# Kernel tuning notes

Hardware: AMD Instinct MI355X
Metric: run time of the kernel (lower is better)

## Reference

```python
import jax, jax.numpy as jnp
import numpy as np

DIM = 1024
HEADS = 16
HD = DIM // HEADS            # 64
MLP = 4 * DIM                # 4096
IN_OUT = MLP + 3 * DIM       # 7168, in_proj out dim
OUT_IN = MLP + DIM           # 5120, out_proj in dim
OUT_OUT = 2 * DIM            # 2048, out_proj out dim
R = 2                        # residual PQ levels
K = 64                       # codebook size
NCB = HEADS                  # num_codebooks = num_heads * codebooks_ratio
IN_CLUSTERS = HEADS * (IN_OUT // DIM)                 # 112
OUT_CLUSTERS = HEADS * max(1, OUT_OUT // OUT_IN)      # 16
SUB_IN = DIM // NCB          # 64
SUB_OUT = OUT_IN // NCB      # 320
EPS = 1e-5


def setup_inputs() -> dict:
    key = jax.random.key(0)
    k1, k2, k3, k4, k5 = jax.random.split(key, 5)
    B, N = 4, 1024
    x = jax.random.normal(k1, (B, N, DIM), jnp.float32)
    in_codebooks = jax.random.normal(k2, (R, IN_CLUSTERS, NCB, K, SUB_IN), jnp.float32) * 0.02
    in_indices = jax.random.randint(k3, (R, IN_OUT, NCB), 0, K, jnp.int32)
    out_codebooks = jax.random.normal(k4, (R, OUT_CLUSTERS, NCB, K, SUB_OUT), jnp.float32) * 0.02
    out_indices = jax.random.randint(k5, (R, OUT_OUT, NCB), 0, K, jnp.int32)
    return {"x": x, "in_codebooks": in_codebooks, "in_indices": in_indices,
            "out_codebooks": out_codebooks, "out_indices": out_indices}


def _decode_weight(cb, idx):
    """Decode RPQ weight. cb: (R, n_clusters, n_codebooks, K, sub), idx: (R, O, n_codebooks).
    Returns dense weight (O, n_codebooks*sub)."""
    Rr, nclust, C, _, sub = cb.shape
    O = idx.shape[1]
    cluster = jnp.arange(O) // (O // nclust)                       # per-row cluster id
    w = cb[jnp.arange(Rr)[:, None, None],
           cluster[None, :, None],
           jnp.arange(C)[None, None, :],
           idx]                                                    # (R, O, C, sub)
    return w.sum(0).reshape(O, C * sub)


def reference(x, in_codebooks, in_indices, out_codebooks, out_indices):
    B, N, C = x.shape
    res = x
    # LayerNorm without affine
    mu = x.mean(-1, keepdims=True)
    var = x.var(-1, keepdims=True)
    xn = (x - mu) * jax.lax.rsqrt(var + EPS)
    # in_proj: dequant + GEMM
    Win = _decode_weight(in_codebooks, in_indices)                 # (IN_OUT, DIM)
    h = jnp.einsum('bnc,oc->bno', xn, Win)                         # (B, N, IN_OUT)
    xm, q, k, v = jnp.split(h, [MLP, MLP + DIM, MLP + 2 * DIM], axis=-1)
    q = q.reshape(B, N, HEADS, HD).transpose(0, 2, 1, 3)
    k = k.reshape(B, N, HEADS, HD).transpose(0, 2, 1, 3)
    v = v.reshape(B, N, HEADS, HD).transpose(0, 2, 1, 3)
    scale = HD ** -0.5
    attn = jax.nn.softmax(jnp.einsum('bhqd,bhkd->bhqk', q, k) * scale, axis=-1)
    xa = jnp.einsum('bhqk,bhkd->bhqd', attn, v).transpose(0, 2, 1, 3).reshape(B, N, C)
    # out_proj: dequant + GEMM on concatenated [mlp, attn]
    Wout = _decode_weight(out_codebooks, out_indices)              # (OUT_OUT, OUT_IN)
    o = jnp.einsum('bnc,oc->bno', jnp.concatenate([xm, xa], axis=-1), Wout)
    x_mlp, x_attn = o[..., :DIM], o[..., DIM:]
    return x_mlp + x_attn + res
```

## Files before the change

### kernel.cpp

```cpp
#include <hip/hip_runtime.h>
#include <hip/hip_bf16.h>

typedef float f32x4 __attribute__((ext_vector_type(4)));
typedef short short8 __attribute__((ext_vector_type(8)));

#define LDH 7168
#define MFMA16(d, x, y) d = __builtin_amdgcn_mfma_f32_16x16x32_bf16(x, y, d, 0, 0, 0)

__device__ __forceinline__ void async_ld16(const void* g, void* l) {
  __builtin_amdgcn_global_load_lds(
      (const __attribute__((address_space(1))) unsigned int*)g,
      (__attribute__((address_space(3))) unsigned int*)l, 16, 0, 0);
}

__device__ __forceinline__ float bf2f(unsigned short u) {
  union { unsigned int i; float f; } c; c.i = ((unsigned int)u) << 16; return c.f;
}

__device__ __forceinline__ ushort4 pack_bf16x4(float4 v) {
  ushort4 u;
  __hip_bfloat16 b;
  b = __float2bfloat16(v.x); u.x = *(unsigned short*)&b;
  b = __float2bfloat16(v.y); u.y = *(unsigned short*)&b;
  b = __float2bfloat16(v.z); u.z = *(unsigned short*)&b;
  b = __float2bfloat16(v.w); u.w = *(unsigned short*)&b;
  return u;
}

__global__ __launch_bounds__(256) void decode_win_k(const float* __restrict__ cb,
                                                    const int* __restrict__ idx,
                                                    __hip_bfloat16* __restrict__ Win) {
  const int o = blockIdx.x;
  const int cluster = o >> 6;
  const int c = threadIdx.x >> 4;
  const int s4 = (threadIdx.x & 15) * 4;
  const int k0 = idx[o * 16 + c];
  const int k1 = idx[(7168 + o) * 16 + c];
  const float4 v0 = *(const float4*)&cb[((((size_t)cluster) * 16 + c) * 64 + k0) * 64 + s4];
  const float4 v1 = *(const float4*)&cb[((((size_t)(112 + cluster)) * 16 + c) * 64 + k1) * 64 + s4];
  float4 v; v.x = v0.x + v1.x; v.y = v0.y + v1.y; v.z = v0.z + v1.z; v.w = v0.w + v1.w;
  *(ushort4*)&Win[(size_t)o * 1024 + c * 64 + s4] = pack_bf16x4(v);
}

__global__ __launch_bounds__(256) void decode_weff_k(const float* __restrict__ cb,
                                                     const int* __restrict__ idx,
                                                     __hip_bfloat16* __restrict__ W) {
  const int o = blockIdx.x;
  const int cl1 = o >> 7, cl2 = cl1 + 8;
  for (int e4 = threadIdx.x * 4; e4 < 5120; e4 += 1024) {
    const int c = e4 / 320, s = e4 - c * 320;
    float4 acc = {0.f, 0.f, 0.f, 0.f};
    #pragma unroll
    for (int r = 0; r < 2; ++r) {
      const int ka = idx[((size_t)r * 2048 + o) * 16 + c];
      const int kb = idx[((size_t)r * 2048 + o + 1024) * 16 + c];
      const float4 va = *(const float4*)&cb[((((size_t)r * 16 + cl1) * 16 + c) * 64 + ka) * 320 + s];
      const float4 vb = *(const float4*)&cb[((((size_t)r * 16 + cl2) * 16 + c) * 64 + kb) * 320 + s];
      acc.x += va.x + vb.x; acc.y += va.y + vb.y; acc.z += va.z + vb.z; acc.w += va.w + vb.w;
    }
    *(ushort4*)&W[(size_t)o * 5120 + e4] = pack_bf16x4(acc);
  }
}

__global__ __launch_bounds__(256) void ln_k(const float* __restrict__ x,
                                            __hip_bfloat16* __restrict__ xn) {
  const int row = blockIdx.x;
  const float4 v = ((const float4*)(x + (size_t)row * 1024))[threadIdx.x];
  float s = v.x + v.y + v.z + v.w;
  float s2 = v.x * v.x + v.y * v.y + v.z * v.z + v.w * v.w;
  #pragma unroll
  for (int off = 32; off > 0; off >>= 1) {
    s += __shfl_down(s, off, 64);
    s2 += __shfl_down(s2, off, 64);
  }
  __shared__ float red[8];
  if ((threadIdx.x & 63) == 0) { red[threadIdx.x >> 6] = s; red[4 + (threadIdx.x >> 6)] = s2; }
  __syncthreads();
  s = red[0] + red[1] + red[2] + red[3];
  s2 = red[4] + red[5] + red[6] + red[7];
  const float mu = s * (1.f / 1024.f);
  const float rstd = rsqrtf(s2 * (1.f / 1024.f) - mu * mu + 1e-5f);
  float4 nv;
  nv.x = (v.x - mu) * rstd; nv.y = (v.y - mu) * rstd;
  nv.z = (v.z - mu) * rstd; nv.w = (v.w - mu) * rstd;
  *(ushort4*)(xn + (size_t)row * 1024 + threadIdx.x * 4) = pack_bf16x4(nv);
}

__global__ __launch_bounds__(512, 2) void gemm1_k(const __hip_bfloat16* __restrict__ A,
                                                  const __hip_bfloat16* __restrict__ B,
                                                  __hip_bfloat16* __restrict__ C,
                                                  __hip_bfloat16* __restrict__ vT) {
  __shared__ ushort sm[65536];
  const int tid = threadIdx.x;
  const int lane = tid & 63, wid = tid >> 6;
  const int g = lane >> 4, r16 = lane & 15;
  const int wr = wid >> 2, wc = wid & 3;

  const int x = blockIdx.x & 7, local = blockIdx.x >> 3;
  const int mb = (x >> 1) * 4 + local / 14;
  const int nb = (x & 1) * 14 + local % 14;
  const int m0 = mb * 256, n0 = nb * 256;

  auto stageA = [&](int kt, int base) {
    #pragma unroll
    for (int i = 0; i < 4; ++i) {
      const int c = i * 512 + tid;
      const int lc = c ^ (((c >> 5) & 1) << 1);
      const int row = lc >> 3, col = (lc & 7) * 8;
      async_ld16(&A[(size_t)(m0 + row) * 1024 + kt * 64 + col], &sm[base + c * 8]);
    }
  };
  auto stageB = [&](int kt, int base) {
    #pragma unroll
    for (int i = 0; i < 4; ++i) {
      const int c = i * 512 + tid;
      const int lc = c ^ (((c >> 5) & 1) << 1);
      const int row = lc >> 3, col = (lc & 7) * 8;
      async_ld16(&B[(size_t)(n0 + row) * 1024 + kt * 64 + col], &sm[base + 16384 + c * 8]);
    }
  };
  auto rdA = [&](int base, int mm, int kk) -> short8 {
    const int row = wr * 128 + mm * 16 + r16;
    int e = row * 64 + kk * 32 + g * 8;
    e ^= ((row >> 2) & 1) << 4;
    return *(const short8*)&sm[base + e];
  };
  auto rdB = [&](int base, int nn, int kk) -> short8 {
    const int row = wc * 64 + nn * 16 + r16;
    int e = row * 64 + kk * 32 + g * 8;
    e ^= ((row >> 2) & 1) << 4;
    return *(const short8*)&sm[base + 16384 + e];
  };

  f32x4 acc[8][4] = {};

  stageA(0, 0); stageB(0, 0);
  asm volatile("s_waitcnt vmcnt(0)" ::: "memory");
  __builtin_amdgcn_s_barrier();
  __builtin_amdgcn_sched_barrier(0);

  auto tile_body = [&](int kt, int base, int nbase) {
    short8 a0[4][2], a1[4][2], b0[2][2], b1[2][2];
    #pragma unroll
    for (int mm = 0; mm < 4; ++mm) { a0[mm][0] = rdA(base, mm, 0); a0[mm][1] = rdA(base, mm, 1); }
    #pragma unroll
    for (int nn = 0; nn < 2; ++nn) { b0[nn][0] = rdB(base, nn, 0); b0[nn][1] = rdB(base, nn, 1); }
    if (kt + 1 < 16) stageA(kt + 1, nbase);
    __builtin_amdgcn_s_setprio(1);
    #pragma unroll
    for (int mm = 0; mm < 4; ++mm)
      #pragma unroll
      for (int nn = 0; nn < 2; ++nn) {
        MFMA16(acc[mm][nn], a0[mm][0], b0[nn][0]);
        MFMA16(acc[mm][nn], a0[mm][1], b0[nn][1]);
      }
    __builtin_amdgcn_s_setprio(0);
    __builtin_amdgcn_s_barrier();
    #pragma unroll
    for (int nn = 0; nn < 2; ++nn) { b1[nn][0] = rdB(base, 2 + nn, 0); b1[nn][1] = rdB(base, 2 + nn, 1); }
    if (kt + 1 < 16) stageB(kt + 1, nbase);
    __builtin_amdgcn_s_setprio(1);
    #pragma unroll
    for (int mm = 0; mm < 4; ++mm)
      #pragma unroll
      for (int nn = 0; nn < 2; ++nn) {
        MFMA16(acc[mm][2 + nn], a0[mm][0], b1[nn][0]);
        MFMA16(acc[mm][2 + nn], a0[mm][1], b1[nn][1]);
      }
    __builtin_amdgcn_s_setprio(0);
    __builtin_amdgcn_s_barrier();
    #pragma unroll
    for (int mm = 0; mm < 4; ++mm) { a1[mm][0] = rdA(base, 4 + mm, 0); a1[mm][1] = rdA(base, 4 + mm, 1); }
    __builtin_amdgcn_s_setprio(1);
    #pragma unroll
    for (int mm = 0; mm < 4; ++mm)
      #pragma unroll
      for (int nn = 0; nn < 2; ++nn) {
        MFMA16(acc[4 + mm][2 + nn], a1[mm][0], b1[nn][0]);
        MFMA16(acc[4 + mm][2 + nn], a1[mm][1], b1[nn][1]);
      }
    __builtin_amdgcn_s_setprio(0);
    __builtin_amdgcn_s_barrier();
    __builtin_amdgcn_s_setprio(1);
    #pragma unroll
    for (int mm = 0; mm < 4; ++mm)
      #pragma unroll
      for (int nn = 0; nn < 2; ++nn) {
        MFMA16(acc[4 + mm][nn], a1[mm][0], b0[nn][0]);
        MFMA16(acc[4 + mm][nn], a1[mm][1], b0[nn][1]);
      }
    __builtin_amdgcn_s_setprio(0);
    asm volatile("s_waitcnt vmcnt(0) lgkmcnt(0)" ::: "memory");
    __builtin_amdgcn_s_barrier();
    __builtin_amdgcn_sched_barrier(0);
  };

  for (int kt = 0; kt < 16; kt += 2) {
    tile_body(kt, 0, 32768);
    tile_body(kt + 1, 32768, 0);
  }

  if (n0 < 6144) {
    #pragma unroll
    for (int mm = 0; mm < 8; ++mm)
      #pragma unroll
      for (int nn = 0; nn < 4; ++nn)
        #pragma unroll
        for (int r = 0; r < 4; ++r) {
          const int m = m0 + wr * 128 + mm * 16 + g * 4 + r;
          const int o = n0 + wc * 64 + nn * 16 + r16;
          C[(size_t)m * LDH + o] = __float2bfloat16(acc[mm][nn][r]);
        }
  } else {
    #pragma unroll
    for (int mm = 0; mm < 8; ++mm)
      #pragma unroll
      for (int nn = 0; nn < 4; ++nn)
        #pragma unroll
        for (int r = 0; r < 4; ++r) {
          const int m = m0 + wr * 128 + mm * 16 + g * 4 + r;
          const int o = n0 + wc * 64 + nn * 16 + r16;
          const int b_ = m >> 10;
          vT[((size_t)b_ * 1024 + (o - 6144)) * 1024 + (m & 1023)] = __float2bfloat16(acc[mm][nn][r]);
        }
  }
}

__global__ __launch_bounds__(256) void attn_k(const __hip_bfloat16* __restrict__ h,
                                              const __hip_bfloat16* __restrict__ vT,
                                              __hip_bfloat16* __restrict__ po0,
                                              __hip_bfloat16* __restrict__ po1,
                                              float* __restrict__ lbuf) {
  const int qt = blockIdx.x & 15, kvs = blockIdx.x >> 4;
  const int head = blockIdx.y, b = blockIdx.z;
  const int tid = threadIdx.x;
  const int lane = tid & 63, w = tid >> 6;
  const int g = lane >> 4, r16 = lane & 15;

  __shared__ __align__(16) __hip_bfloat16 Ks[2][64 * 64];
  __shared__ __align__(16) __hip_bfloat16 Vs[2][64 * 64];
  __shared__ __align__(16) __hip_bfloat16 P[4][16][72];

  const __hip_bfloat16* Kg = h + (size_t)(b * 1024) * LDH + 5120 + head * 64;
  const __hip_bfloat16* Vg = vT + ((size_t)b * 1024 + head * 64) * 1024;

  const size_t qrow = (size_t)(b * 1024 + qt * 64 + w * 16 + r16);
  short8 aq0 = *(const short8*)&h[qrow * LDH + 4096 + head * 64 + g * 8];
  short8 aq1 = *(const short8*)&h[qrow * LDH + 4096 + head * 64 + 32 + g * 8];

  auto stage = [&](int buf, int t) {
    #pragma unroll
    for (int i = 0; i < 2; ++i) {
      const int c_lin = i * 256 + tid;
      const int row = c_lin >> 3;
      const int c_log = (c_lin & 7) ^ (row & 7);
      async_ld16(&Kg[(size_t)(t * 64 + row) * LDH + c_log * 8], &Ks[buf][c_lin * 8]);
    }
    #pragma unroll
    for (int i = 0; i < 2; ++i) {
      const int c_lin = i * 256 + tid;
      const int row = c_lin >> 3;
      const int c_log = (c_lin & 7) ^ (row & 7);
      async_ld16(&Vg[(size_t)row * 1024 + t * 64 + c_log * 8], &Vs[buf][c_lin * 8]);
    }
  };

  f32x4 o_acc[4] = {};
  float l_r[4] = {0.f, 0.f, 0.f, 0.f};

  const int t0 = kvs * 8;
  stage(0, t0);
  for (int tt = 0; tt < 8; ++tt) {
    const int buf = tt & 1;
    if (tt + 1 < 8) {
      stage(buf ^ 1, t0 + tt + 1);
      asm volatile("s_waitcnt vmcnt(4)" ::: "memory");
    } else {
      asm volatile("s_waitcnt vmcnt(0)" ::: "memory");
    }
    __builtin_amdgcn_s_barrier();
    __builtin_amdgcn_sched_barrier(0);

    f32x4 s_acc[4] = {};
    #pragma unroll
    for (int nn = 0; nn < 4; ++nn) {
      const int row = nn * 16 + r16;
      short8 bk0 = *(const short8*)&Ks[buf][row * 64 + ((g ^ (row & 7)) * 8)];
      short8 bk1 = *(const short8*)&Ks[buf][row * 64 + (((g + 4) ^ (row & 7)) * 8)];
      s_acc[nn] = __builtin_amdgcn_mfma_f32_16x16x32_bf16(aq0, bk0, s_acc[nn], 0, 0, 0);
      s_acc[nn] = __builtin_amdgcn_mfma_f32_16x16x32_bf16(aq1, bk1, s_acc[nn], 0, 0, 0);
    }

    #pragma unroll
    for (int nn = 0; nn < 4; ++nn)
      #pragma unroll
      for (int r = 0; r < 4; ++r) {
        const float p = __expf(s_acc[nn][r] * 0.125f);
        s_acc[nn][r] = p;
        l_r[r] += p;
      }

    #pragma unroll
    for (int nn = 0; nn < 4; ++nn)
      #pragma unroll
      for (int r = 0; r < 4; ++r)
        P[w][g * 4 + r][nn * 16 + r16] = __float2bfloat16(s_acc[nn][r]);
    short8 ap0 = *(const short8*)&P[w][r16][g * 8];
    short8 ap1 = *(const short8*)&P[w][r16][32 + g * 8];

    #pragma unroll
    for (int nn = 0; nn < 4; ++nn) {
      const int row = nn * 16 + r16;
      short8 bv0 = *(const short8*)&Vs[buf][row * 64 + ((g ^ (row & 7)) * 8)];
      short8 bv1 = *(const short8*)&Vs[buf][row * 64 + (((g + 4) ^ (row & 7)) * 8)];
      o_acc[nn] = __builtin_amdgcn_mfma_f32_16x16x32_bf16(ap0, bv0, o_acc[nn], 0, 0, 0);
      o_acc[nn] = __builtin_amdgcn_mfma_f32_16x16x32_bf16(ap1, bv1, o_acc[nn], 0, 0, 0);
    }
    __builtin_amdgcn_s_barrier();
    __builtin_amdgcn_sched_barrier(0);
  }

  __hip_bfloat16* po = kvs ? po1 : po0;
  #pragma unroll
  for (int r = 0; r < 4; ++r) {
    float l = l_r[r];
    #pragma unroll
    for (int off = 1; off < 16; off <<= 1) l += __shfl_xor(l, off, 64);
    const size_t mrow = (size_t)(b * 1024 + qt * 64 + w * 16 + g * 4 + r);
    #pragma unroll
    for (int nn = 0; nn < 4; ++nn)
      po[mrow * 1024 + head * 64 + nn * 16 + r16] = __float2bfloat16(o_acc[nn][r]);
    if (r16 == 0) lbuf[(mrow * 16 + head) * 2 + kvs] = l;
  }
}

__global__ __launch_bounds__(256) void combine_k(const __hip_bfloat16* __restrict__ po0,
                                                 const float* __restrict__ lbuf,
                                                 __hip_bfloat16* __restrict__ xa) {
  const int row = blockIdx.x;
  const int e4 = threadIdx.x * 4;
  const int head = e4 >> 6;
  const float l = lbuf[(((size_t)row) * 16 + head) * 2 + 0]
                + lbuf[(((size_t)row) * 16 + head) * 2 + 1];
  const float inv = 1.0f / l;
  const ushort4 a = *(const ushort4*)&po0[(size_t)row * 1024 + e4];
  const ushort4 bb = *(const ushort4*)&xa[(size_t)row * 1024 + e4];
  float4 v;
  v.x = (bf2f(a.x) + bf2f(bb.x)) * inv;
  v.y = (bf2f(a.y) + bf2f(bb.y)) * inv;
  v.z = (bf2f(a.z) + bf2f(bb.z)) * inv;
  v.w = (bf2f(a.w) + bf2f(bb.w)) * inv;
  *(ushort4*)&xa[(size_t)row * 1024 + e4] = pack_bf16x4(v);
}

__global__ __launch_bounds__(512, 2) void gemm2_k(const __hip_bfloat16* __restrict__ h,
                                                  const __hip_bfloat16* __restrict__ xa,
                                                  const __hip_bfloat16* __restrict__ W,
                                                  __hip_bfloat16* __restrict__ p0,
                                                  __hip_bfloat16* __restrict__ p1,
                                                  __hip_bfloat16* __restrict__ p2,
                                                  float* __restrict__ out) {
  __shared__ ushort sm[65536];
  const int tid = threadIdx.x;
  const int lane = tid & 63, wid = tid >> 6;
  const int g = lane >> 4, r16 = lane & 15;
  const int wr = wid >> 2, wc = wid & 3;

  int bid = blockIdx.x;
  bid = (bid & 7) * 8 + (bid >> 3);
  const int mb = bid >> 2, nb = bid & 3;
  const int m0 = mb * 256, n0 = nb * 256;
  const int z = blockIdx.y;
  const int kt0 = z * 20, ktEnd = kt0 + 20;

  auto stageA = [&](int kt, int base) {
    const __hip_bfloat16* Ab; size_t lda; int kc;
    if (kt < 64) { Ab = h;  lda = LDH;  kc = kt * 64; }
    else         { Ab = xa; lda = 1024; kc = kt * 64 - 4096; }
    #pragma unroll
    for (int i = 0; i < 4; ++i) {
      const int c = i * 512 + tid;
      const int lc = c ^ (((c >> 5) & 1) << 1);
      const int row = lc >> 3, col = (lc & 7) * 8;
      async_ld16(&Ab[(size_t)(m0 + row) * lda + kc + col], &sm[base + c * 8]);
    }
  };
  auto stageB = [&](int kt, int base) {
    #pragma unroll
    for (int i = 0; i < 4; ++i) {
      const int c = i * 512 + tid;
      const int lc = c ^ (((c >> 5) & 1) << 1);
      const int row = lc >> 3, col = (lc & 7) * 8;
      async_ld16(&W[(size_t)(n0 + row) * 5120 + kt * 64 + col], &sm[base + 16384 + c * 8]);
    }
  };
  auto rdA = [&](int base, int mm, int kk) -> short8 {
    const int row = wr * 128 + mm * 16 + r16;
    int e = row * 64 + kk * 32 + g * 8;
    e ^= ((row >> 2) & 1) << 4;
    return *(const short8*)&sm[base + e];
  };
  auto rdB = [&](int base, int nn, int kk) -> short8 {
    const int row = wc * 64 + nn * 16 + r16;
    int e = row * 64 + kk * 32 + g * 8;
    e ^= ((row >> 2) & 1) << 4;
    return *(const short8*)&sm[base + 16384 + e];
  };

  f32x4 acc[8][4] = {};

  stageA(kt0, 0); stageB(kt0, 0);
  asm volatile("s_waitcnt vmcnt(0)" ::: "memory");
  __builtin_amdgcn_s_barrier();
  __builtin_amdgcn_sched_barrier(0);

  auto tile_body = [&](int kt, int base, int nbase) {
    short8 a0[4][2], a1[4][2], b0[2][2], b1[2][2];
    #pragma unroll
    for (int mm = 0; mm < 4; ++mm) { a0[mm][0] = rdA(base, mm, 0); a0[mm][1] = rdA(base, mm, 1); }
    #pragma unroll
    for (int nn = 0; nn < 2; ++nn) { b0[nn][0] = rdB(base, nn, 0); b0[nn][1] = rdB(base, nn, 1); }
    if (kt + 1 < ktEnd) stageA(kt + 1, nbase);
    __builtin_amdgcn_s_setprio(1);
    #pragma unroll
    for (int mm = 0; mm < 4; ++mm)
      #pragma unroll
      for (int nn = 0; nn < 2; ++nn) {
        MFMA16(acc[mm][nn], a0[mm][0], b0[nn][0]);
        MFMA16(acc[mm][nn], a0[mm][1], b0[nn][1]);
      }
    __builtin_amdgcn_s_setprio(0);
    __builtin_amdgcn_s_barrier();
    #pragma unroll
    for (int nn = 0; nn < 2; ++nn) { b1[nn][0] = rdB(base, 2 + nn, 0); b1[nn][1] = rdB(base, 2 + nn, 1); }
    if (kt + 1 < ktEnd) stageB(kt + 1, nbase);
    __builtin_amdgcn_s_setprio(1);
    #pragma unroll
    for (int mm = 0; mm < 4; ++mm)
      #pragma unroll
      for (int nn = 0; nn < 2; ++nn) {
        MFMA16(acc[mm][2 + nn], a0[mm][0], b1[nn][0]);
        MFMA16(acc[mm][2 + nn], a0[mm][1], b1[nn][1]);
      }
    __builtin_amdgcn_s_setprio(0);
    __builtin_amdgcn_s_barrier();
    #pragma unroll
    for (int mm = 0; mm < 4; ++mm) { a1[mm][0] = rdA(base, 4 + mm, 0); a1[mm][1] = rdA(base, 4 + mm, 1); }
    __builtin_amdgcn_s_setprio(1);
    #pragma unroll
    for (int mm = 0; mm < 4; ++mm)
      #pragma unroll
      for (int nn = 0; nn < 2; ++nn) {
        MFMA16(acc[4 + mm][2 + nn], a1[mm][0], b1[nn][0]);
        MFMA16(acc[4 + mm][2 + nn], a1[mm][1], b1[nn][1]);
      }
    __builtin_amdgcn_s_setprio(0);
    __builtin_amdgcn_s_barrier();
    __builtin_amdgcn_s_setprio(1);
    #pragma unroll
    for (int mm = 0; mm < 4; ++mm)
      #pragma unroll
      for (int nn = 0; nn < 2; ++nn) {
        MFMA16(acc[4 + mm][nn], a1[mm][0], b0[nn][0]);
        MFMA16(acc[4 + mm][nn], a1[mm][1], b0[nn][1]);
      }
    __builtin_amdgcn_s_setprio(0);
    asm volatile("s_waitcnt vmcnt(0) lgkmcnt(0)" ::: "memory");
    __builtin_amdgcn_s_barrier();
    __builtin_amdgcn_sched_barrier(0);
  };

  for (int kt = kt0; kt < ktEnd; kt += 2) {
    tile_body(kt, 0, 32768);
    tile_body(kt + 1, 32768, 0);
  }

  __hip_bfloat16* pz = (z == 0) ? p0 : (z == 1) ? p1 : p2;
  #pragma unroll
  for (int mm = 0; mm < 8; ++mm)
    #pragma unroll
    for (int nn = 0; nn < 4; ++nn)
      #pragma unroll
      for (int r = 0; r < 4; ++r) {
        const int m = m0 + wr * 128 + mm * 16 + g * 4 + r;
        const int n = n0 + wc * 64 + nn * 16 + r16;
        if (z == 3) out[(size_t)m * 1024 + n] = acc[mm][nn][r];
        else        pz[(size_t)m * 1024 + n] = __float2bfloat16(acc[mm][nn][r]);
      }
}

__global__ __launch_bounds__(256) void reduce_k(const __hip_bfloat16* __restrict__ p0,
                                                const __hip_bfloat16* __restrict__ p1,
                                                const __hip_bfloat16* __restrict__ p2,
                                                const float* __restrict__ res,
                                                float* __restrict__ out) {
  const size_t i4 = (size_t)blockIdx.x * 256 + threadIdx.x;
  float4 o = ((const float4*)out)[i4];
  const float4 rr = ((const float4*)res)[i4];
  const ushort4 a0 = ((const ushort4*)p0)[i4];
  const ushort4 a1 = ((const ushort4*)p1)[i4];
  const ushort4 a2 = ((const ushort4*)p2)[i4];
  o.x += rr.x + bf2f(a0.x) + bf2f(a1.x) + bf2f(a2.x);
  o.y += rr.y + bf2f(a0.y) + bf2f(a1.y) + bf2f(a2.y);
  o.z += rr.z + bf2f(a0.z) + bf2f(a1.z) + bf2f(a2.z);
  o.w += rr.w + bf2f(a0.w) + bf2f(a1.w) + bf2f(a2.w);
  ((float4*)out)[i4] = o;
}

extern "C" void kernel_launch(void* const* d_in, const int* in_sizes, int n_in,
                              void* d_out, int out_size, void* d_ws, size_t ws_size,
                              hipStream_t stream) {
  (void)in_sizes; (void)n_in; (void)out_size; (void)ws_size;
  const float* x      = (const float*)d_in[0];
  const float* in_cb  = (const float*)d_in[1];
  const int*   in_idx = (const int*)d_in[2];
  const float* out_cb = (const float*)d_in[3];
  const int*   out_idx= (const int*)d_in[4];
  float* out = (float*)d_out;
  char* ws = (char*)d_ws;

  __hip_bfloat16* Win  = (__hip_bfloat16*)(ws);
  __hip_bfloat16* Weff = (__hip_bfloat16*)(ws + 14680064);
  __hip_bfloat16* xn   = (__hip_bfloat16*)(ws + 25165824);
  __hip_bfloat16* h    = (__hip_bfloat16*)(ws + 33554432);
  __hip_bfloat16* vT   = (__hip_bfloat16*)(ws + 92274688);
  __hip_bfloat16* xa   = (__hip_bfloat16*)(ws + 100663296);

  __hip_bfloat16* po0  = Win;
  float*          lbuf = (float*)xn;
  __hip_bfloat16* pk0 = Win;
  __hip_bfloat16* pk1 = xn;
  __hip_bfloat16* pk2 = vT;

  decode_win_k<<<dim3(7168), dim3(256), 0, stream>>>(in_cb, in_idx, Win);
  decode_weff_k<<<dim3(1024), dim3(256), 0, stream>>>(out_cb, out_idx, Weff);
  ln_k<<<dim3(4096), dim3(256), 0, stream>>>(x, xn);
  gemm1_k<<<dim3(448), dim3(512), 0, stream>>>(xn, Win, h, vT);
  attn_k<<<dim3(32, 16, 4), dim3(256), 0, stream>>>(h, vT, po0, xa, lbuf);
  combine_k<<<dim3(4096), dim3(256), 0, stream>>>(po0, lbuf, xa);
  gemm2_k<<<dim3(64, 4), dim3(512), 0, stream>>>(h, xa, Weff, pk0, pk1, pk2, out);
  reduce_k<<<dim3(4096), dim3(256), 0, stream>>>(pk0, pk1, pk2, x, out);
}
```

Measured before the change: 202.9 us.

## Merge decode and layernorm kernels; split attention KV into four chunks

Three preprocessing kernels (Win decode, Weff decode, layernorm) are merged into one launch that dispatches on block index, removing two launches and their tail gaps. Attention now splits the KV range into four chunks instead of two, doubling the grid to 4096 blocks for better occupancy. Two extra partial-output buffers are placed in the output buffer, and lbuf stores four partial sums per row. The combine kernel reads four partials, which adds memory traffic and makes more bf16 partial roundings.

```diff
diff --git a/kernel.cpp b/kernel.cpp
--- a/kernel.cpp
+++ b/kernel.cpp
@@ -27,63 +27,64 @@
   return u;
 }
 
-__global__ __launch_bounds__(256) void decode_win_k(const float* __restrict__ cb,
-                                                    const int* __restrict__ idx,
-                                                    __hip_bfloat16* __restrict__ Win) {
-  const int o = blockIdx.x;
-  const int cluster = o >> 6;
-  const int c = threadIdx.x >> 4;
-  const int s4 = (threadIdx.x & 15) * 4;
-  const int k0 = idx[o * 16 + c];
-  const int k1 = idx[(7168 + o) * 16 + c];
-  const float4 v0 = *(const float4*)&cb[((((size_t)cluster) * 16 + c) * 64 + k0) * 64 + s4];
-  const float4 v1 = *(const float4*)&cb[((((size_t)(112 + cluster)) * 16 + c) * 64 + k1) * 64 + s4];
-  float4 v; v.x = v0.x + v1.x; v.y = v0.y + v1.y; v.z = v0.z + v1.z; v.w = v0.w + v1.w;
-  *(ushort4*)&Win[(size_t)o * 1024 + c * 64 + s4] = pack_bf16x4(v);
-}
-
-__global__ __launch_bounds__(256) void decode_weff_k(const float* __restrict__ cb,
-                                                     const int* __restrict__ idx,
-                                                     __hip_bfloat16* __restrict__ W) {
-  const int o = blockIdx.x;
-  const int cl1 = o >> 7, cl2 = cl1 + 8;
-  for (int e4 = threadIdx.x * 4; e4 < 5120; e4 += 1024) {
-    const int c = e4 / 320, s = e4 - c * 320;
-    float4 acc = {0.f, 0.f, 0.f, 0.f};
-    #pragma unroll
-    for (int r = 0; r < 2; ++r) {
-      const int ka = idx[((size_t)r * 2048 + o) * 16 + c];
-      const int kb = idx[((size_t)r * 2048 + o + 1024) * 16 + c];
-      const float4 va = *(const float4*)&cb[((((size_t)r * 16 + cl1) * 16 + c) * 64 + ka) * 320 + s];
-      const float4 vb = *(const float4*)&cb[((((size_t)r * 16 + cl2) * 16 + c) * 64 + kb) * 320 + s];
-      acc.x += va.x + vb.x; acc.y += va.y + vb.y; acc.z += va.z + vb.z; acc.w += va.w + vb.w;
-    }
-    *(ushort4*)&W[(size_t)o * 5120 + e4] = pack_bf16x4(acc);
+__global__ __launch_bounds__(256) void prep_k(const float* __restrict__ x,
+                                              const float* __restrict__ in_cb,
+                                              const int* __restrict__ in_idx,
+                                              const float* __restrict__ out_cb,
+                                              const int* __restrict__ out_idx,
+                                              __hip_bfloat16* __restrict__ Win,
+                                              __hip_bfloat16* __restrict__ Weff,
+                                              __hip_bfloat16* __restrict__ xn) {
+  const int bid = blockIdx.x;
+  if (bid < 7168) {
+    const int o = bid;
+    const int cluster = o >> 6;
+    const int c = threadIdx.x >> 4;
+    const int s4 = (threadIdx.x & 15) * 4;
+    const int k0 = in_idx[o * 16 + c];
+    const int k1 = in_idx[(7168 + o) * 16 + c];
+    const float4 v0 = *(const float4*)&in_cb[((((size_t)cluster) * 16 + c) * 64 + k0) * 64 + s4];
+    const float4 v1 = *(const float4*)&in_cb[((((size_t)(112 + cluster)) * 16 + c) * 64 + k1) * 64 + s4];
+    float4 v; v.x = v0.x + v1.x; v.y = v0.y + v1.y; v.z = v0.z + v1.z; v.w = v0.w + v1.w;
+    *(ushort4*)&Win[(size_t)o * 1024 + c * 64 + s4] = pack_bf16x4(v);
+  } else if (bid < 8192) {
+    const int o = bid - 7168;
+    const int cl1 = o >> 7, cl2 = cl1 + 8;
+    for (int e4 = threadIdx.x * 4; e4 < 5120; e4 += 1024) {
+      const int c = e4 / 320, s = e4 - c * 320;
+      float4 acc = {0.f, 0.f, 0.f, 0.f};
+      #pragma unroll
+      for (int r = 0; r < 2; ++r) {
+        const int ka = out_idx[((size_t)r * 2048 + o) * 16 + c];
+        const int kb = out_idx[((size_t)r * 2048 + o + 1024) * 16 + c];
+        const float4 va = *(const float4*)&out_cb[((((size_t)r * 16 + cl1) * 16 + c) * 64 + ka) * 320 + s];
+        const float4 vb = *(const float4*)&out_cb[((((size_t)r * 16 + cl2) * 16 + c) * 64 + kb) * 320 + s];
+        acc.x += va.x + vb.x; acc.y += va.y + vb.y; acc.z += va.z + vb.z; acc.w += va.w + vb.w;
+      }
+      *(ushort4*)&Weff[(size_t)o * 5120 + e4] = pack_bf16x4(acc);
+    }
+  } else {
+    const int row = bid - 8192;
+    const float4 v = ((const float4*)(x + (size_t)row * 1024))[threadIdx.x];
+    float s = v.x + v.y + v.z + v.w;
+    float s2 = v.x * v.x + v.y * v.y + v.z * v.z + v.w * v.w;
+    #pragma unroll
+    for (int off = 32; off > 0; off >>= 1) {
+      s += __shfl_down(s, off, 64);
+      s2 += __shfl_down(s2, off, 64);
+    }
+    __shared__ float red[8];
+    if ((threadIdx.x & 63) == 0) { red[threadIdx.x >> 6] = s; red[4 + (threadIdx.x >> 6)] = s2; }
+    __syncthreads();
+    s = red[0] + red[1] + red[2] + red[3];
+    s2 = red[4] + red[5] + red[6] + red[7];
+    const float mu = s * (1.f / 1024.f);
+    const float rstd = rsqrtf(s2 * (1.f / 1024.f) - mu * mu + 1e-5f);
+    float4 nv;
+    nv.x = (v.x - mu) * rstd; nv.y = (v.y - mu) * rstd;
+    nv.z = (v.z - mu) * rstd; nv.w = (v.w - mu) * rstd;
+    *(ushort4*)(xn + (size_t)row * 1024 + threadIdx.x * 4) = pack_bf16x4(nv);
   }
-}
-
-__global__ __launch_bounds__(256) void ln_k(const float* __restrict__ x,
-                                            __hip_bfloat16* __restrict__ xn) {
-  const int row = blockIdx.x;
-  const float4 v = ((const float4*)(x + (size_t)row * 1024))[threadIdx.x];
-  float s = v.x + v.y + v.z + v.w;
-  float s2 = v.x * v.x + v.y * v.y + v.z * v.z + v.w * v.w;
-  #pragma unroll
-  for (int off = 32; off > 0; off >>= 1) {
-    s += __shfl_down(s, off, 64);
-    s2 += __shfl_down(s2, off, 64);
-  }
-  __shared__ float red[8];
-  if ((threadIdx.x & 63) == 0) { red[threadIdx.x >> 6] = s; red[4 + (threadIdx.x >> 6)] = s2; }
-  __syncthreads();
-  s = red[0] + red[1] + red[2] + red[3];
-  s2 = red[4] + red[5] + red[6] + red[7];
-  const float mu = s * (1.f / 1024.f);
-  const float rstd = rsqrtf(s2 * (1.f / 1024.f) - mu * mu + 1e-5f);
-  float4 nv;
-  nv.x = (v.x - mu) * rstd; nv.y = (v.y - mu) * rstd;
-  nv.z = (v.z - mu) * rstd; nv.w = (v.w - mu) * rstd;
-  *(ushort4*)(xn + (size_t)row * 1024 + threadIdx.x * 4) = pack_bf16x4(nv);
 }
 
 __global__ __launch_bounds__(512, 2) void gemm1_k(const __hip_bfloat16* __restrict__ A,
@@ -230,6 +231,8 @@
                                               const __hip_bfloat16* __restrict__ vT,
                                               __hip_bfloat16* __restrict__ po0,
                                               __hip_bfloat16* __restrict__ po1,
+                                              __hip_bfloat16* __restrict__ po2,
+                                              __hip_bfloat16* __restrict__ po3,
                                               float* __restrict__ lbuf) {
   const int qt = blockIdx.x & 15, kvs = blockIdx.x >> 4;
   const int head = blockIdx.y, b = blockIdx.z;
@@ -268,11 +271,11 @@
   f32x4 o_acc[4] = {};
   float l_r[4] = {0.f, 0.f, 0.f, 0.f};
 
-  const int t0 = kvs * 8;
+  const int t0 = kvs * 4;
   stage(0, t0);
-  for (int tt = 0; tt < 8; ++tt) {
+  for (int tt = 0; tt < 4; ++tt) {
     const int buf = tt & 1;
-    if (tt + 1 < 8) {
+    if (tt + 1 < 4) {
       stage(buf ^ 1, t0 + tt + 1);
       asm volatile("s_waitcnt vmcnt(4)" ::: "memory");
     } else {
@@ -320,7 +323,7 @@
     __builtin_amdgcn_sched_barrier(0);
   }
 
-  __hip_bfloat16* po = kvs ? po1 : po0;
+  __hip_bfloat16* po = (kvs == 0) ? po0 : (kvs == 1) ? po1 : (kvs == 2) ? po2 : po3;
   #pragma unroll
   for (int r = 0; r < 4; ++r) {
     float l = l_r[r];
@@ -330,26 +333,29 @@
     #pragma unroll
     for (int nn = 0; nn < 4; ++nn)
       po[mrow * 1024 + head * 64 + nn * 16 + r16] = __float2bfloat16(o_acc[nn][r]);
-    if (r16 == 0) lbuf[(mrow * 16 + head) * 2 + kvs] = l;
+    if (r16 == 0) lbuf[(mrow * 16 + head) * 4 + kvs] = l;
   }
 }
 
 __global__ __launch_bounds__(256) void combine_k(const __hip_bfloat16* __restrict__ po0,
+                                                 const __hip_bfloat16* __restrict__ po2,
+                                                 const __hip_bfloat16* __restrict__ po3,
                                                  const float* __restrict__ lbuf,
                                                  __hip_bfloat16* __restrict__ xa) {
   const int row = blockIdx.x;
   const int e4 = threadIdx.x * 4;
   const int head = e4 >> 6;
-  const float l = lbuf[(((size_t)row) * 16 + head) * 2 + 0]
-                + lbuf[(((size_t)row) * 16 + head) * 2 + 1];
-  const float inv = 1.0f / l;
+  const float* lb = &lbuf[(((size_t)row) * 16 + head) * 4];
+  const float inv = 1.0f / (lb[0] + lb[1] + lb[2] + lb[3]);
   const ushort4 a = *(const ushort4*)&po0[(size_t)row * 1024 + e4];
   const ushort4 bb = *(const ushort4*)&xa[(size_t)row * 1024 + e4];
+  const ushort4 c = *(const ushort4*)&po2[(size_t)row * 1024 + e4];
+  const ushort4 d = *(const ushort4*)&po3[(size_t)row * 1024 + e4];
   float4 v;
-  v.x = (bf2f(a.x) + bf2f(bb.x)) * inv;
-  v.y = (bf2f(a.y) + bf2f(bb.y)) * inv;
-  v.z = (bf2f(a.z) + bf2f(bb.z)) * inv;
-  v.w = (bf2f(a.w) + bf2f(bb.w)) * inv;
+  v.x = (bf2f(a.x) + bf2f(bb.x) + bf2f(c.x) + bf2f(d.x)) * inv;
+  v.y = (bf2f(a.y) + bf2f(bb.y) + bf2f(c.y) + bf2f(d.y)) * inv;
+  v.z = (bf2f(a.z) + bf2f(bb.z) + bf2f(c.z) + bf2f(d.z)) * inv;
+  v.w = (bf2f(a.w) + bf2f(bb.w) + bf2f(c.w) + bf2f(d.w)) * inv;
   *(ushort4*)&xa[(size_t)row * 1024 + e4] = pack_bf16x4(v);
 }
 
@@ -527,17 +533,17 @@
   __hip_bfloat16* xa   = (__hip_bfloat16*)(ws + 100663296);
 
   __hip_bfloat16* po0  = Win;
+  __hip_bfloat16* po2  = (__hip_bfloat16*)out;
+  __hip_bfloat16* po3  = (__hip_bfloat16*)out + 4194304;
   float*          lbuf = (float*)xn;
   __hip_bfloat16* pk0 = Win;
   __hip_bfloat16* pk1 = xn;
   __hip_bfloat16* pk2 = vT;
 
-  decode_win_k<<<dim3(7168), dim3(256), 0, stream>>>(in_cb, in_idx, Win);
-  decode_weff_k<<<dim3(1024), dim3(256), 0, stream>>>(out_cb, out_idx, Weff);
-  ln_k<<<dim3(4096), dim3(256), 0, stream>>>(x, xn);
+  prep_k<<<dim3(12288), dim3(256), 0, stream>>>(x, in_cb, in_idx, out_cb, out_idx, Win, Weff, xn);
   gemm1_k<<<dim3(448), dim3(512), 0, stream>>>(xn, Win, h, vT);
-  attn_k<<<dim3(32, 16, 4), dim3(256), 0, stream>>>(h, vT, po0, xa, lbuf);
-  combine_k<<<dim3(4096), dim3(256), 0, stream>>>(po0, lbuf, xa);
+  attn_k<<<dim3(64, 16, 4), dim3(256), 0, stream>>>(h, vT, po0, xa, po2, po3, lbuf);
+  combine_k<<<dim3(4096), dim3(256), 0, stream>>>(po0, po2, po3, lbuf, xa);
   gemm2_k<<<dim3(64, 4), dim3(512), 0, stream>>>(h, xa, Weff, pk0, pk1, pk2, out);
   reduce_k<<<dim3(4096), dim3(256), 0, stream>>>(pk0, pk1, pk2, x, out);
 }
```

Measured after the change: 203.4 us (median of 2 runs). About the same (+0.3%).
